# Kernel tuning notes

Hardware: AMD Instinct MI355X
Metric: run time of the kernel (lower is better)

Reference implementation:

```python
import jax, jax.numpy as jnp
import numpy as np

B, S, M, D, F, H = 1, 2048, 512, 1024, 4096, 16
DH = D // H
W = 256  # Longformer half-window: query attends to keys within +/-W global positions


def layer_norm(x, g, b, eps=1e-5):
    mu = jnp.mean(x, axis=-1, keepdims=True)
    var = jnp.var(x, axis=-1, keepdims=True)
    return (x - mu) * jax.lax.rsqrt(var + eps) * g + b


def rel_sinusoid(dists, d_model):
    # Transformer-XL sinusoidal embedding of (possibly negative) relative distances
    inv_freq = 1.0 / (10000.0 ** (jnp.arange(0, d_model, 2, dtype=jnp.float32) / d_model))
    ang = dists[:, None].astype(jnp.float32) * inv_freq[None, :]
    return jnp.concatenate([jnp.sin(ang), jnp.cos(ang)], axis=-1)  # [nR, D]


def setup_inputs() -> dict:
    key = jax.random.key(0)
    ks = jax.random.split(key, 18)
    sc = D ** -0.5
    inp = {
        "x": jax.random.normal(ks[0], (B, S, D), jnp.float32),
        "mem": jax.random.normal(ks[1], (B, M, D), jnp.float32),
        "Wq": jax.random.normal(ks[2], (D, D), jnp.float32) * sc,
        "Wk": jax.random.normal(ks[3], (D, D), jnp.float32) * sc,
        "Wv": jax.random.normal(ks[4], (D, D), jnp.float32) * sc,
        "Wo": jax.random.normal(ks[5], (D, D), jnp.float32) * sc,
        "Wr": jax.random.normal(ks[6], (D, D), jnp.float32) * sc,
        "u": jax.random.normal(ks[7], (H, DH), jnp.float32) * 0.02,
        "v": jax.random.normal(ks[8], (H, DH), jnp.float32) * 0.02,
        "ln1_g": jnp.ones((D,), jnp.float32),
        "ln1_b": jnp.zeros((D,), jnp.float32),
        "W1": jax.random.normal(ks[9], (D, F), jnp.float32) * sc,
        "b1": jnp.zeros((F,), jnp.float32),
        "W2": jax.random.normal(ks[10], (F, D), jnp.float32) * (F ** -0.5),
        "b2": jnp.zeros((D,), jnp.float32),
        "ln2_g": jnp.ones((D,), jnp.float32),
        "ln2_b": jnp.zeros((D,), jnp.float32),
    }
    return inp


def reference(x, mem, Wq, Wk, Wv, Wo, Wr, u, v, ln1_g, ln1_b, W1, b1, W2, b2, ln2_g, ln2_b):
    L = M + S  # key/value length after prepending XL memory
    kv = jnp.concatenate([mem, x], axis=1)  # [B, L, D]
    q = (x @ Wq).reshape(B, S, H, DH)
    k = (kv @ Wk).reshape(B, L, H, DH)
    vv = (kv @ Wv).reshape(B, L, H, DH)

    # relative distances: global query pos = M+i, key pos = j -> dist = M+i-j in [-(S-1), M+S-1]
    dists = jnp.arange(-(S - 1), M + S)  # [nR]
    R = (rel_sinusoid(dists, D) @ Wr).reshape(-1, H, DH)  # [nR, H, DH]

    AC = jnp.einsum("bqhd,blhd->bhql", q + u, k)          # content term
    BD_all = jnp.einsum("bqhd,rhd->bhqr", q + v, R)        # position term per distance
    qi = jnp.arange(S)[:, None]
    kj = jnp.arange(L)[None, :]
    dist = M + qi - kj                                       # [S, L]
    idx = dist + (S - 1)
    BD = jnp.take_along_axis(BD_all, jnp.broadcast_to(idx[None, None], (B, H, S, L)), axis=-1)

    scores = (AC + BD) * (DH ** -0.5)
    band = jnp.abs(dist) <= W                                # sliding-window (banded) mask
    scores = jnp.where(band[None, None], scores, -1e30)
    attn = jax.nn.softmax(scores, axis=-1)
    o = jnp.einsum("bhql,blhd->bqhd", attn, vv).reshape(B, S, D) @ Wo

    h = layer_norm(x + o, ln1_g, ln1_b)                      # residual + LN (dropout: eval mode)
    f = jax.nn.gelu(h @ W1 + b1) @ W2 + b2                   # FFN
    return layer_norm(h + f, ln2_g, ln2_b)
```

## Files before the change

### kernel.cpp

```cpp
#include <hip/hip_runtime.h>
#include <hip/hip_bf16.h>
#include <cstdint>

#define S_ 2048
#define M_ 512
#define L_ 2560
#define D_ 1024
#define F_ 4096
#define H_ 16
#define DH_ 64
#define W_ 256
#define NR_ 513
#define NRP_ 640

typedef unsigned int uint32;
typedef __attribute__((ext_vector_type(8))) short bf16x8;
typedef __attribute__((ext_vector_type(4))) float f32x4;

__device__ __forceinline__ ushort f2bf(float f) {
  uint32 u = __builtin_bit_cast(uint32, f);
  u += 0x7FFFu + ((u >> 16) & 1u);
  return (ushort)(u >> 16);
}
__device__ __forceinline__ float bf2f(ushort s) {
  uint32 u = ((uint32)s) << 16;
  return __builtin_bit_cast(float, u);
}
__device__ __forceinline__ ushort4 pack4(float4 vf) {
  ushort4 r;
  r.x = f2bf(vf.x); r.y = f2bf(vf.y); r.z = f2bf(vf.z); r.w = f2bf(vf.w);
  return r;
}
__device__ __forceinline__ float gelu_tanh(float x) {
  float t = 0.7978845608028654f * x * (1.f + 0.044715f * x * x);
  float e = __expf(2.f * t);
  float th = 1.f - 2.f / (e + 1.f);
  return 0.5f * x * (1.f + th);
}

__device__ __forceinline__ void gld_lds16(const ushort* g, ushort* l) {
  __builtin_amdgcn_global_load_lds((const __attribute__((address_space(1))) void*)g,
                                   (__attribute__((address_space(3))) void*)l, 16, 0, 0);
}

__device__ __forceinline__ void tr_tile(const float* __restrict__ in, ushort* __restrict__ out,
                                        int R, int C, int c0, int r0, int tx, int ty,
                                        float (*tile)[33]) {
#pragma unroll
  for (int i = 0; i < 4; i++)
    tile[ty + i * 8][tx] = in[(size_t)(r0 + ty + i * 8) * C + c0 + tx];
  __syncthreads();
#pragma unroll
  for (int i = 0; i < 4; i++)
    out[(size_t)(c0 + ty + i * 8) * R + r0 + tx] = f2bf(tile[tx][ty + i * 8]);
}

__global__ __launch_bounds__(256)
void prep_kernel(const float* __restrict__ x, const float* __restrict__ mem,
                 const float* __restrict__ Wq, const float* __restrict__ Wk,
                 const float* __restrict__ Wv, const float* __restrict__ Wo,
                 const float* __restrict__ Wr, const float* __restrict__ W1,
                 const float* __restrict__ W2,
                 ushort* __restrict__ WqT, ushort* __restrict__ WkT,
                 ushort* __restrict__ WvT, ushort* __restrict__ WoT,
                 ushort* __restrict__ WrT, ushort* __restrict__ W1T,
                 ushort* __restrict__ W2T,
                 ushort* __restrict__ kvb, ushort* __restrict__ remb) {
  __shared__ float tile[32][33];
  const int bid = blockIdx.x;
  const int tid = threadIdx.x;
  const int tx = tid & 31, ty = tid >> 5;

  if (bid < 5120) {
    const int which = bid >> 10, idx = bid & 1023;
    const float* ins[5] = {Wq, Wk, Wv, Wo, Wr};
    ushort* outs[5] = {WqT, WkT, WvT, WoT, WrT};
    tr_tile(ins[which], outs[which], 1024, 1024, (idx & 31) * 32, (idx >> 5) * 32, tx, ty, tile);
  } else if (bid < 9216) {
    const int idx = bid - 5120;
    tr_tile(W1, W1T, 1024, 4096, (idx % 128) * 32, (idx / 128) * 32, tx, ty, tile);
  } else if (bid < 13312) {
    const int idx = bid - 9216;
    tr_tile(W2, W2T, 4096, 1024, (idx & 31) * 32, (idx >> 5) * 32, tx, ty, tile);
  } else if (bid < 15872) {
    const int k = (bid - 13312) * 256 + tid;
    const int l = k >> 8, c = k & 255;
    const float4* src = (l < M_) ? (const float4*)(mem + (size_t)l * D_)
                                 : (const float4*)(x + (size_t)(l - M_) * D_);
    ((ushort4*)kvb)[k] = pack4(src[c]);
  } else {
    const int idx = (bid - 15872) * 256 + tid;
    const int r = idx >> 9, f = idx & 511;
    if (r < NR_) {
      float invf = expf(-(float)f * (9.210340371976184f / 512.0f));
      float ang = (float)(r - W_) * invf;
      remb[(size_t)r * D_ + f] = f2bf(sinf(ang));
      remb[(size_t)r * D_ + 512 + f] = f2bf(cosf(ang));
    } else if (r < NRP_) {
      remb[(size_t)r * D_ + f] = 0;
      remb[(size_t)r * D_ + 512 + f] = 0;
    }
  }
}

template <int EPI, int SPLITK>
__device__ __forceinline__
void gemm8p2_core(const ushort* __restrict__ A, const ushort* __restrict__ BT,
                  void* __restrict__ Cout, void* __restrict__ Cout2,
                  void* __restrict__ Cout3, void* __restrict__ Cout4,
                  const float* __restrict__ bias, int Msz, int Nsz, int Ksz, int Kstride,
                  int gx, int bid, int nwg, char* dyn) {
  const int tid = threadIdx.x;
  const int wave = tid >> 6, lane = tid & 63;
  const int wr = wave >> 2, wc = wave & 3;
  const int fr = lane & 15, gf = lane >> 4;
  const int sl = fr & 7;

  const int xcd = bid & 7, idx = bid >> 3;
  const int q = nwg >> 3, r8 = nwg & 7;
  const int swz = (xcd < r8 ? xcd * (q + 1) : r8 * (q + 1) + (xcd - r8) * q) + idx;
  const int gy = Msz / 128;
  const int bx = swz % gx;
  const int rest = swz / gx;
  const int by = rest % gy;
  const int bz = rest / gy;
  const int brow = by * 128, bcol = bx * 256;
  const int koff = (SPLITK > 1) ? bz * Ksz : 0;

  const int nt = Ksz >> 6;

  const int srow = tid >> 3;
  const int scol = ((tid & 7) ^ (srow & 7)) * 8;
  const ushort* Ab = A + (size_t)(brow + srow) * Kstride + koff + scol;
  const ushort* Bb = BT + (size_t)(bcol + srow) * Kstride + koff + scol;

  auto stageA = [&](int t, int qm) {
    gld_lds16(Ab + (size_t)(qm * 64) * Kstride + t * 64,
              (ushort*)(dyn + (t & 1) * 49152 + qm * 8192) + wave * 512);
  };
  auto stageB = [&](int t, int qn) {
#pragma unroll
    for (int j = 0; j < 2; j++)
      gld_lds16(Bb + (size_t)(qn * 128 + j * 64) * Kstride + t * 64,
                (ushort*)(dyn + (t & 1) * 49152 + 16384 + qn * 16384 + j * 8192) + wave * 512);
  };

  const int ar0 = (wr * 32 + fr) * 128;
  const int ar1 = (wr * 32 + 16 + fr) * 128;
  const int br0 = (wc * 32 + fr) * 128;
  const int br1 = (wc * 32 + 16 + fr) * 128;
  const int s0 = (gf ^ sl) * 16;
  const int s1 = ((4 + gf) ^ sl) * 16;

  f32x4 acc00[2][2] = {}, acc01[2][2] = {}, acc10[2][2] = {}, acc11[2][2] = {};

  stageA(0, 0); stageB(0, 0); stageB(0, 1); stageA(0, 1);
  stageA(1, 0); stageB(1, 0);
  asm volatile("s_waitcnt vmcnt(3)" ::: "memory");
  __builtin_amdgcn_s_barrier();
  __builtin_amdgcn_sched_barrier(0);

#define PH4(QM, QN, ACC, STAGES, WAITS)                                                 \
  {                                                                                     \
    const char* ab = dyn + cur * 49152 + (QM) * 8192;                                   \
    const char* bb = dyn + cur * 49152 + 16384 + (QN) * 16384;                          \
    bf16x8 a00 = *(const bf16x8*)(ab + ar0 + s0);                                       \
    bf16x8 a10 = *(const bf16x8*)(ab + ar1 + s0);                                       \
    bf16x8 a01 = *(const bf16x8*)(ab + ar0 + s1);                                       \
    bf16x8 a11 = *(const bf16x8*)(ab + ar1 + s1);                                       \
    bf16x8 b00 = *(const bf16x8*)(bb + br0 + s0);                                       \
    bf16x8 b10 = *(const bf16x8*)(bb + br1 + s0);                                       \
    bf16x8 b01 = *(const bf16x8*)(bb + br0 + s1);                                       \
    bf16x8 b11 = *(const bf16x8*)(bb + br1 + s1);                                       \
    STAGES;                                                                             \
    WAITS;                                                                              \
    __builtin_amdgcn_s_barrier();                                                       \
    asm volatile("s_waitcnt lgkmcnt(0)" ::: "memory");                                  \
    __builtin_amdgcn_sched_barrier(0);                                                  \
    __builtin_amdgcn_s_setprio(1);                                                      \
    ACC[0][0] = __builtin_amdgcn_mfma_f32_16x16x32_bf16(a00, b00, ACC[0][0], 0, 0, 0);  \
    ACC[0][1] = __builtin_amdgcn_mfma_f32_16x16x32_bf16(a00, b10, ACC[0][1], 0, 0, 0);  \
    ACC[1][0] = __builtin_amdgcn_mfma_f32_16x16x32_bf16(a10, b00, ACC[1][0], 0, 0, 0);  \
    ACC[1][1] = __builtin_amdgcn_mfma_f32_16x16x32_bf16(a10, b10, ACC[1][1], 0, 0, 0);  \
    ACC[0][0] = __builtin_amdgcn_mfma_f32_16x16x32_bf16(a01, b01, ACC[0][0], 0, 0, 0);  \
    ACC[0][1] = __builtin_amdgcn_mfma_f32_16x16x32_bf16(a01, b11, ACC[0][1], 0, 0, 0);  \
    ACC[1][0] = __builtin_amdgcn_mfma_f32_16x16x32_bf16(a11, b01, ACC[1][0], 0, 0, 0);  \
    ACC[1][1] = __builtin_amdgcn_mfma_f32_16x16x32_bf16(a11, b11, ACC[1][1], 0, 0, 0);  \
    __builtin_amdgcn_s_setprio(0);                                                      \
    __builtin_amdgcn_s_barrier();                                                       \
  }

  for (int t = 0; t < nt; t++) {
    const int cur = t & 1;
    PH4(0, 0, acc00, { if (t + 1 < nt) stageB(t + 1, 1); }, {});
    PH4(0, 1, acc01, { if (t + 1 < nt) stageA(t + 1, 1); }, {});
    PH4(1, 0, acc10, { if (t + 2 < nt) stageA(t + 2, 0); }, {});
    PH4(1, 1, acc11, { if (t + 2 < nt) stageB(t + 2, 0); },
        {
          if (t + 1 < nt) {
            if (t + 2 < nt) asm volatile("s_waitcnt vmcnt(3)" ::: "memory");
            else            asm volatile("s_waitcnt vmcnt(0)" ::: "memory");
          }
        });
  }
#undef PH4

  const int r4 = gf * 4;
  float* co = (float*)Cout;
  bool addb = (EPI == 3);
  if constexpr (SPLITK >= 2) {
    if (bz == 1) { co = (float*)Cout2; addb = false; }
  }
  if constexpr (SPLITK == 4) {
    if (bz == 2) { co = (float*)Cout3; addb = false; }
    if (bz == 3) { co = (float*)Cout4; addb = false; }
  }
  auto wrq = [&](const f32x4 (&ACC)[2][2], int QM, int QN) {
#pragma unroll
    for (int m = 0; m < 2; m++) {
#pragma unroll
      for (int n = 0; n < 2; n++) {
        const int col = bcol + QN * 128 + wc * 32 + n * 16 + fr;
        const int row0 = brow + QM * 64 + wr * 32 + m * 16 + r4;
        if constexpr (EPI == 5) {
          if (col < 1024) {
#pragma unroll
            for (int r = 0; r < 4; r++)
              ((ushort*)Cout)[(size_t)(row0 + r) * 1024 + col] = f2bf(ACC[m][n][r]);
          } else {
            ushort4 pk;
            pk.x = f2bf(ACC[m][n][0]); pk.y = f2bf(ACC[m][n][1]);
            pk.z = f2bf(ACC[m][n][2]); pk.w = f2bf(ACC[m][n][3]);
            *(ushort4*)((ushort*)Cout2 + (size_t)(col - 1024) * Msz + row0) = pk;
          }
        } else if constexpr (EPI == 0 || EPI == 2) {
#pragma unroll
          for (int r = 0; r < 4; r++) {
            float val = ACC[m][n][r];
            size_t o = (size_t)(row0 + r) * Nsz + col;
            if constexpr (EPI == 2) ((ushort*)Cout)[o] = f2bf(gelu_tanh(val + bias[col]));
            else ((ushort*)Cout)[o] = f2bf(val);
          }
        } else {
#pragma unroll
          for (int r = 0; r < 4; r++) {
            float val = ACC[m][n][r];
            co[(size_t)(row0 + r) * Nsz + col] = addb ? val + bias[col] : val;
          }
        }
      }
    }
  };
  wrq(acc00, 0, 0);
  wrq(acc01, 0, 1);
  wrq(acc10, 1, 0);
  wrq(acc11, 1, 1);
}

template <int EPI, int SPLITK>
__global__ __launch_bounds__(512)
void gemm8p2_kern(const ushort* __restrict__ A, const ushort* __restrict__ BT,
                  void* __restrict__ Cout, void* __restrict__ Cout2,
                  void* __restrict__ Cout3, void* __restrict__ Cout4,
                  const float* __restrict__ bias, int Msz, int Nsz, int Ksz, int Kstride,
                  int gx) {
  extern __shared__ __align__(16) char dyn[];
  gemm8p2_core<EPI, SPLITK>(A, BT, Cout, Cout2, Cout3, Cout4, bias,
                            Msz, Nsz, Ksz, Kstride, gx, blockIdx.x, gridDim.x, dyn);
}

__global__ __launch_bounds__(512)
void proj8p(const ushort* __restrict__ kvb, const ushort* __restrict__ WqT,
            const ushort* __restrict__ WkvT, const ushort* __restrict__ WrT,
            const ushort* __restrict__ remb,
            ushort* __restrict__ qb, ushort* __restrict__ kb,
            ushort* __restrict__ Vt, ushort* __restrict__ Rb) {
  extern __shared__ __align__(16) char dyn[];
  const int bid = blockIdx.x;
  if (bid < 64) {
    gemm8p2_core<0, 1>(kvb + 512 * 1024, WqT, qb, nullptr, nullptr, nullptr, nullptr,
                       2048, 1024, 1024, 1024, 4, bid, 64, dyn);
  } else if (bid < 224) {
    gemm8p2_core<5, 1>(kvb, WkvT, kb, Vt, nullptr, nullptr, nullptr,
                       2560, 2048, 1024, 1024, 8, bid - 64, 160, dyn);
  } else {
    gemm8p2_core<0, 1>(remb, WrT, Rb, nullptr, nullptr, nullptr, nullptr,
                       640, 1024, 1024, 1024, 4, bid - 224, 20, dyn);
  }
}

__global__ __launch_bounds__(256)
void attn_mfma5(const ushort* __restrict__ qb, const ushort* __restrict__ kb,
                const ushort* __restrict__ Vt, const ushort* __restrict__ Rb,
                const float* __restrict__ ubias, const float* __restrict__ vbias,
                ushort* __restrict__ attb) {
  const int bid = blockIdx.x;
  const int swz = (bid & 7) * 64 + (bid >> 3);
  const int h = swz >> 5;
  const int i0 = (swz & 31) * 64;
  const int tid = threadIdx.x;
  const int wave = tid >> 6, lane = tid & 63;
  const int g = lane >> 4, fr = lane & 15;
  const int hD = h * DH_;

  __shared__ __align__(16) ushort ring[4][16][128];
  __shared__ __align__(16) ushort Pl[4][16][40];

  const int qi = i0 + wave * 16 + fr;
  bf16x8 afu[2], afv[2];
#pragma unroll
  for (int kst = 0; kst < 2; kst++) {
    const int dof = kst * 32 + g * 8;
    bf16x8 qv = *(const bf16x8*)(qb + (size_t)qi * D_ + hD + dof);
    const float* up = ubias + hD + dof;
    const float* vp = vbias + hD + dof;
    bf16x8 au, av;
#pragma unroll
    for (int j = 0; j < 8; j++) {
      float q = bf2f((ushort)qv[j]);
      au[j] = (short)f2bf(q + up[j]);
      av[j] = (short)f2bf(q + vp[j]);
    }
    afu[kst] = au; afv[kst] = av;
  }

  const int jb = 256 + i0;
  const int smax = 2303 - i0;
  const int sbase = wave * 16;

  auto produce = [&](int r0, bf16x8 rf0, bf16x8 rf1) {
    f32x4 acc = {};
    __builtin_amdgcn_s_setprio(1);
    acc = __builtin_amdgcn_mfma_f32_16x16x32_bf16(afv[0], rf0, acc, 0, 0, 0);
    acc = __builtin_amdgcn_mfma_f32_16x16x32_bf16(afv[1], rf1, acc, 0, 0, 0);
    __builtin_amdgcn_s_setprio(0);
#pragma unroll
    for (int rr = 0; rr < 4; rr++)
      ring[wave][g * 4 + rr][(r0 + fr) & 127] = f2bf(acc[rr]);
  };
  auto loadRrow = [&](int row, bf16x8* out0, bf16x8* out1) {
    const int rc = row < 0 ? 0 : row;
    *out0 = *(const bf16x8*)(Rb + (size_t)rc * D_ + hD + g * 8);
    *out1 = *(const bf16x8*)(Rb + (size_t)rc * D_ + hD + 32 + g * 8);
  };
  auto loadK = [&](int ch, bf16x8 (&kp)[2][2]) {
#pragma unroll
    for (int half = 0; half < 2; half++) {
      const int sa = sbase + ch * 32 + half * 16 + fr;
      const int jc = (jb + sa < L_ - 1) ? (jb + sa) : (L_ - 1);
      kp[half][0] = *(const bf16x8*)(kb + (size_t)jc * 1024 + hD + g * 8);
      kp[half][1] = *(const bf16x8*)(kb + (size_t)jc * 1024 + hD + 32 + g * 8);
    }
  };
  auto loadV = [&](int ch, bf16x8 (&vp)[4]) {
    int kc = jb + sbase + ch * 32 + g * 8;
    if (kc > L_ - 8) kc = L_ - 8;
#pragma unroll
    for (int n = 0; n < 4; n++)
      vp[n] = *(const bf16x8*)(Vt + (size_t)(hD + n * 16 + fr) * L_ + kc);
  };

#pragma unroll
  for (int t = 0; t < 3; t++) {
    const int r0 = 480 + t * 16;
    bf16x8 rf0, rf1;
    loadRrow(r0 + fr, &rf0, &rf1);
    produce(r0, rf0, rf1);
  }

  float m4[4], l4[4];
  f32x4 oacc[4] = {};
#pragma unroll
  for (int rr = 0; rr < 4; rr++) { m4[rr] = -1e30f; l4[rr] = 0.f; }

  bf16x8 kA[2][2], vA[4], kB[2][2], vB[4];
  bf16x8 rA[4], rB[4];
  loadRrow(448 + fr, &rA[0], &rA[1]);
  loadRrow(464 + fr, &rA[2], &rA[3]);
  loadK(0, kA); loadV(0, vA);

  auto body = [&](int ch, bf16x8 (&kU)[2][2], bf16x8 (&vU)[4],
                  bf16x8 (&kP)[2][2], bf16x8 (&vP)[4],
                  bf16x8 (&rU)[4], bf16x8 (&rP)[4], bool first) -> bool {
    const int c0 = sbase + ch * 32;
    if (c0 > smax) return false;
    f32x4 sc[2];
#pragma unroll
    for (int half = 0; half < 2; half++) {
      f32x4 acc = {};
      __builtin_amdgcn_s_setprio(1);
      acc = __builtin_amdgcn_mfma_f32_16x16x32_bf16(afu[0], kU[half][0], acc, 0, 0, 0);
      acc = __builtin_amdgcn_mfma_f32_16x16x32_bf16(afu[1], kU[half][1], acc, 0, 0, 0);
      __builtin_amdgcn_s_setprio(0);
      sc[half] = acc;
    }
    if (ch < 16) {
      loadK(ch + 1, kP);
      loadV(ch + 1, vP);
    }
    if (ch < 15) {
      loadRrow(416 - ch * 32 + fr, &rP[0], &rP[1]);
      loadRrow(432 - ch * 32 + fr, &rP[2], &rP[3]);
    }
#pragma unroll
    for (int half = 0; half < 2; half++) {
      const int rb2 = 512 + g * 4 - (ch * 32 + half * 16 + fr);
      const int sa = c0 + half * 16 + fr;
#pragma unroll
      for (int rr = 0; rr < 4; rr++) {
        const int r = rb2 + rr;
        const float bd = bf2f(ring[wave][g * 4 + rr][r & 127]);
        const bool valid = ((unsigned)r <= 512u) && (sa <= smax);
        sc[half][rr] = valid ? (sc[half][rr] + bd) * 0.125f : -1e30f;
      }
    }
    if (first) {
      f32x4 cm;
#pragma unroll
      for (int rr = 0; rr < 4; rr++) cm[rr] = fmaxf(sc[0][rr], sc[1][rr]);
#pragma unroll
      for (int off = 8; off; off >>= 1)
#pragma unroll
        for (int rr = 0; rr < 4; rr++) cm[rr] = fmaxf(cm[rr], __shfl_xor(cm[rr], off));
#pragma unroll
      for (int rr = 0; rr < 4; rr++) m4[rr] = cm[rr];
    } else {
      bool rise = false;
#pragma unroll
      for (int rr = 0; rr < 4; rr++)
        rise |= (fmaxf(sc[0][rr], sc[1][rr]) > m4[rr] + 8.f);
      if (__any(rise)) {
        f32x4 cm;
#pragma unroll
        for (int rr = 0; rr < 4; rr++) cm[rr] = fmaxf(sc[0][rr], sc[1][rr]);
#pragma unroll
        for (int off = 8; off; off >>= 1)
#pragma unroll
          for (int rr = 0; rr < 4; rr++) cm[rr] = fmaxf(cm[rr], __shfl_xor(cm[rr], off));
#pragma unroll
        for (int rr = 0; rr < 4; rr++) {
          const float nm = fmaxf(m4[rr], cm[rr]);
          const float esc = __expf(m4[rr] - nm);
          m4[rr] = nm;
          l4[rr] *= esc;
#pragma unroll
          for (int n = 0; n < 4; n++) oacc[n][rr] *= esc;
        }
      }
    }
    f32x4 pA, pB;
#pragma unroll
    for (int rr = 0; rr < 4; rr++) {
      pA[rr] = __expf(sc[0][rr] - m4[rr]);
      pB[rr] = __expf(sc[1][rr] - m4[rr]);
      l4[rr] += pA[rr] + pB[rr];
    }
#pragma unroll
    for (int rr = 0; rr < 4; rr++) {
      Pl[wave][g * 4 + rr][fr]      = f2bf(pA[rr]);
      Pl[wave][g * 4 + rr][16 + fr] = f2bf(pB[rr]);
    }
    bf16x8 pf = *(const bf16x8*)&Pl[wave][fr][g * 8];
    if (ch < 16) {
      produce(448 - ch * 32, rU[0], rU[1]);
      produce(464 - ch * 32, rU[2], rU[3]);
    }
    __builtin_amdgcn_s_setprio(1);
#pragma unroll
    for (int n = 0; n < 4; n++)
      oacc[n] = __builtin_amdgcn_mfma_f32_16x16x32_bf16(pf, vU[n], oacc[n], 0, 0, 0);
    __builtin_amdgcn_s_setprio(0);
    return true;
  };

  bool cont = body(0, kA, vA, kB, vB, rA, rB, true);
  for (int ch = 1; ch < 17 && cont; ch += 2) {
    cont = body(ch, kB, vB, kA, vA, rB, rA, false);
    if (!cont || ch + 1 >= 17) break;
    cont = body(ch + 1, kA, vA, kB, vB, rA, rB, false);
  }

#pragma unroll
  for (int off = 8; off; off >>= 1)
#pragma unroll
    for (int rr = 0; rr < 4; rr++) l4[rr] += __shfl_xor(l4[rr], off);
#pragma unroll
  for (int rr = 0; rr < 4; rr++) {
    const float inv = 1.f / l4[rr];
    const size_t rowo = (size_t)(i0 + sbase + g * 4 + rr) * D_ + hD;
#pragma unroll
    for (int n = 0; n < 4; n++)
      attb[rowo + n * 16 + fr] = f2bf(oacc[n][rr] * inv);
  }
}

__global__ __launch_bounds__(256)
void ln_kernel(const float* __restrict__ a, const float* __restrict__ b,
               const float* __restrict__ c, const float* __restrict__ d,
               const float* __restrict__ e,
               const float* __restrict__ gamma, const float* __restrict__ beta,
               float* __restrict__ outf, ushort* __restrict__ outb) {
  const int row = blockIdx.x;
  const int tid = threadIdx.x;
  const int wave = tid >> 6, lane = tid & 63;
  float4 va = ((const float4*)(a + (size_t)row * D_))[tid];
  float4 vb4 = ((const float4*)(b + (size_t)row * D_))[tid];
  float4 xv;
  xv.x = va.x + vb4.x; xv.y = va.y + vb4.y; xv.z = va.z + vb4.z; xv.w = va.w + vb4.w;
  if (c) {
    float4 vc = ((const float4*)(c + (size_t)row * D_))[tid];
    xv.x += vc.x; xv.y += vc.y; xv.z += vc.z; xv.w += vc.w;
  }
  if (d) {
    float4 vd = ((const float4*)(d + (size_t)row * D_))[tid];
    xv.x += vd.x; xv.y += vd.y; xv.z += vd.z; xv.w += vd.w;
  }
  if (e) {
    float4 ve = ((const float4*)(e + (size_t)row * D_))[tid];
    xv.x += ve.x; xv.y += ve.y; xv.z += ve.z; xv.w += ve.w;
  }
  float s = xv.x + xv.y + xv.z + xv.w;
  float q = xv.x * xv.x + xv.y * xv.y + xv.z * xv.z + xv.w * xv.w;
#pragma unroll
  for (int off = 32; off; off >>= 1) { s += __shfl_xor(s, off); q += __shfl_xor(q, off); }
  __shared__ float red[8];
  if (lane == 0) { red[wave * 2] = s; red[wave * 2 + 1] = q; }
  __syncthreads();
  float ts = red[0] + red[2] + red[4] + red[6];
  float tq = red[1] + red[3] + red[5] + red[7];
  float mu = ts * (1.f / D_);
  float var = tq * (1.f / D_) - mu * mu;
  float rs = rsqrtf(var + 1e-5f);
  float4 g4 = ((const float4*)gamma)[tid];
  float4 be4 = ((const float4*)beta)[tid];
  float4 y;
  y.x = (xv.x - mu) * rs * g4.x + be4.x;
  y.y = (xv.y - mu) * rs * g4.y + be4.y;
  y.z = (xv.z - mu) * rs * g4.z + be4.z;
  y.w = (xv.w - mu) * rs * g4.w + be4.w;
  ((float4*)(outf + (size_t)row * D_))[tid] = y;
  if (outb) ((ushort4*)(outb + (size_t)row * D_))[tid] = pack4(y);
}

extern "C" void kernel_launch(void* const* d_in, const int* in_sizes, int n_in,
                              void* d_out, int out_size, void* d_ws, size_t ws_size,
                              hipStream_t stream) {
  const float* x    = (const float*)d_in[0];
  const float* mem  = (const float*)d_in[1];
  const float* Wq   = (const float*)d_in[2];
  const float* Wk   = (const float*)d_in[3];
  const float* Wv   = (const float*)d_in[4];
  const float* Wo   = (const float*)d_in[5];
  const float* Wr   = (const float*)d_in[6];
  const float* u    = (const float*)d_in[7];
  const float* v    = (const float*)d_in[8];
  const float* ln1g = (const float*)d_in[9];
  const float* ln1b = (const float*)d_in[10];
  const float* W1   = (const float*)d_in[11];
  const float* b1   = (const float*)d_in[12];
  const float* W2   = (const float*)d_in[13];
  const float* b2   = (const float*)d_in[14];
  const float* ln2g = (const float*)d_in[15];
  const float* ln2b = (const float*)d_in[16];
  float* out = (float*)d_out;

  char* ws = (char*)d_ws;
  size_t off = 0;
  auto take = [&](size_t n) { char* p = ws + off; off += (n + 255) & ~(size_t)255; return p; };

  ushort* WqT = (ushort*)take(2097152);
  ushort* WkT = (ushort*)take(2097152);
  ushort* WvT = (ushort*)take(2097152);
  ushort* WoT = (ushort*)take(2097152);
  ushort* WrT = (ushort*)take(2097152);
  ushort* W1T = (ushort*)take(8388608);
  ushort* W2T = (ushort*)take(8388608);

  char* regA = take(8388608);
  ushort* kvb  = (ushort*)regA;
  ushort* remb = (ushort*)(regA + 5242880);
  float*  fbuf = (float*)regA;

  char* regB = take(20185088);
  ushort* qb   = (ushort*)regB;
  ushort* kb   = (ushort*)(regB + 4194304);
  ushort* Vt   = (ushort*)(regB + 9437184);
  ushort* Rb   = (ushort*)(regB + 14680064);
  ushort* attb = (ushort*)(regB + 15990784);
  float*  o2b  = (float*)regB;
  ushort* g    = (ushort*)regB;

  float*  o2 = (float*)take(8388608);
  float*  h  = (float*)take(8388608);
  ushort* hb = (ushort*)take(4194304);

  float* p2 = (float*)WqT;
  float* p3 = (float*)W1T;

  prep_kernel<<<17152, 256, 0, stream>>>(x, mem, Wq, Wk, Wv, Wo, Wr, W1, W2,
                                         WqT, WkT, WvT, WoT, WrT, W1T, W2T, kvb, remb);

  proj8p<<<244, 512, 98304, stream>>>(kvb, WqT, WkT, WrT, remb, qb, kb, Vt, Rb);

  attn_mfma5<<<512, 256, 0, stream>>>(qb, kb, Vt, Rb, u, v, attb);

  gemm8p2_kern<1, 2><<<128, 512, 98304, stream>>>(attb, WoT, o2, o2b, nullptr, nullptr,
                                                  nullptr, 2048, 1024, 512, 1024, 4);
  ln_kernel<<<2048, 256, 0, stream>>>(x, o2, o2b, nullptr, nullptr, ln1g, ln1b, h, hb);

  gemm8p2_kern<2, 1><<<256, 512, 98304, stream>>>(hb, W1T, g, nullptr, nullptr, nullptr,
                                                  b1, 2048, 4096, 1024, 1024, 16);

  gemm8p2_kern<3, 4><<<256, 512, 98304, stream>>>(g, W2T, fbuf, o2, p2, p3,
                                                  b2, 2048, 1024, 1024, 4096, 4);
  ln_kernel<<<2048, 256, 0, stream>>>(h, fbuf, o2, p2, p3, ln2g, ln2b, out, nullptr);
}
```

Baseline: 187.9 us.

## Split attention key range across two blocks and merge partial softmax results

The banded attention kernel now launches twice as many blocks, each covering half of the key chunks, and writes unnormalized fp32 partial outputs plus running max and sum. A new merge kernel rescales and combines the two halves, normalizes, and emits bf16. The aim is more blocks in flight on a 512-block grid that underfills the GPU, so the serial chunk loop per block gets shorter. The cost is extra fp32 global traffic, a second launch, and a small LDS padding change to the ring buffer.

```diff
diff --git a/kernel.cpp b/kernel.cpp
--- a/kernel.cpp
+++ b/kernel.cpp
@@ -290,12 +290,15 @@
 }
 
 __global__ __launch_bounds__(256)
-void attn_mfma5(const ushort* __restrict__ qb, const ushort* __restrict__ kb,
+void attn_mfma6(const ushort* __restrict__ qb, const ushort* __restrict__ kb,
                 const ushort* __restrict__ Vt, const ushort* __restrict__ Rb,
                 const float* __restrict__ ubias, const float* __restrict__ vbias,
-                ushort* __restrict__ attb) {
+                float* __restrict__ OA, float* __restrict__ OB,
+                float* __restrict__ mlb) {
   const int bid = blockIdx.x;
-  const int swz = (bid & 7) * 64 + (bid >> 3);
+  const int hf = bid >> 9;
+  const int inner = bid & 511;
+  const int swz = (inner & 7) * 64 + (inner >> 3);
   const int h = swz >> 5;
   const int i0 = (swz & 31) * 64;
   const int tid = threadIdx.x;
@@ -303,7 +306,10 @@
   const int g = lane >> 4, fr = lane & 15;
   const int hD = h * DH_;
 
-  __shared__ __align__(16) ushort ring[4][16][128];
+  const int chS = hf ? 9 : 0;
+  const int chE = hf ? 16 : 8;
+
+  __shared__ __align__(16) ushort ring[4][16][136];
   __shared__ __align__(16) ushort Pl[4][16][40];
 
   const int qi = i0 + wave * 16 + fr;
@@ -360,9 +366,10 @@
       vp[n] = *(const bf16x8*)(Vt + (size_t)(hD + n * 16 + fr) * L_ + kc);
   };
 
+  const int base = 480 - chS * 32;
 #pragma unroll
   for (int t = 0; t < 3; t++) {
-    const int r0 = 480 + t * 16;
+    const int r0 = base + t * 16;
     bf16x8 rf0, rf1;
     loadRrow(r0 + fr, &rf0, &rf1);
     produce(r0, rf0, rf1);
@@ -375,9 +382,9 @@
 
   bf16x8 kA[2][2], vA[4], kB[2][2], vB[4];
   bf16x8 rA[4], rB[4];
-  loadRrow(448 + fr, &rA[0], &rA[1]);
-  loadRrow(464 + fr, &rA[2], &rA[3]);
-  loadK(0, kA); loadV(0, vA);
+  loadRrow(base - 32 + fr, &rA[0], &rA[1]);
+  loadRrow(base - 16 + fr, &rA[2], &rA[3]);
+  loadK(chS, kA); loadV(chS, vA);
 
   auto body = [&](int ch, bf16x8 (&kU)[2][2], bf16x8 (&vU)[4],
                   bf16x8 (&kP)[2][2], bf16x8 (&vP)[4],
@@ -394,11 +401,11 @@
       __builtin_amdgcn_s_setprio(0);
       sc[half] = acc;
     }
-    if (ch < 16) {
+    if (ch < chE) {
       loadK(ch + 1, kP);
       loadV(ch + 1, vP);
     }
-    if (ch < 15) {
+    if (ch < chE - 1) {
       loadRrow(416 - ch * 32 + fr, &rP[0], &rP[1]);
       loadRrow(432 - ch * 32 + fr, &rP[2], &rP[3]);
     }
@@ -461,7 +468,7 @@
       Pl[wave][g * 4 + rr][16 + fr] = f2bf(pB[rr]);
     }
     bf16x8 pf = *(const bf16x8*)&Pl[wave][fr][g * 8];
-    if (ch < 16) {
+    if (ch < chE) {
       produce(448 - ch * 32, rU[0], rU[1]);
       produce(464 - ch * 32, rU[2], rU[3]);
     }
@@ -473,10 +480,10 @@
     return true;
   };
 
-  bool cont = body(0, kA, vA, kB, vB, rA, rB, true);
-  for (int ch = 1; ch < 17 && cont; ch += 2) {
+  bool cont = body(chS, kA, vA, kB, vB, rA, rB, true);
+  for (int ch = chS + 1; ch <= chE && cont; ch += 2) {
     cont = body(ch, kB, vB, kA, vA, rB, rA, false);
-    if (!cont || ch + 1 >= 17) break;
+    if (!cont || ch + 1 > chE) break;
     cont = body(ch + 1, kA, vA, kB, vB, rA, rB, false);
   }
 
@@ -484,14 +491,44 @@
   for (int off = 8; off; off >>= 1)
 #pragma unroll
     for (int rr = 0; rr < 4; rr++) l4[rr] += __shfl_xor(l4[rr], off);
+
+  float* Obuf = hf ? OB : OA;
+  float* ml = mlb + (hf ? 65536 : 0);
 #pragma unroll
   for (int rr = 0; rr < 4; rr++) {
-    const float inv = 1.f / l4[rr];
-    const size_t rowo = (size_t)(i0 + sbase + g * 4 + rr) * D_ + hD;
+    const int row = i0 + sbase + g * 4 + rr;
+    const size_t rowo = (size_t)row * D_ + hD;
 #pragma unroll
     for (int n = 0; n < 4; n++)
-      attb[rowo + n * 16 + fr] = f2bf(oacc[n][rr] * inv);
-  }
+      Obuf[rowo + n * 16 + fr] = oacc[n][rr];
+    if (fr == 0) {
+      ml[row * 16 + h] = m4[rr];
+      ml[32768 + row * 16 + h] = l4[rr];
+    }
+  }
+}
+
+__global__ __launch_bounds__(256)
+void attn_merge(const float* __restrict__ OA, const float* __restrict__ OB,
+                const float* __restrict__ mlb, ushort* __restrict__ attb) {
+  const int q = blockIdx.x;
+  const int tid = threadIdx.x;
+  const int h = tid >> 4;
+  const float mA = mlb[q * 16 + h];
+  const float lA = mlb[32768 + q * 16 + h];
+  const float mB = mlb[65536 + q * 16 + h];
+  const float lB = mlb[98304 + q * 16 + h];
+  const float m = fmaxf(mA, mB);
+  const float eA = __expf(mA - m), eB = __expf(mB - m);
+  const float inv = 1.f / (eA * lA + eB * lB);
+  float4 a = ((const float4*)(OA + (size_t)q * 1024))[tid];
+  float4 b = ((const float4*)(OB + (size_t)q * 1024))[tid];
+  ushort4 o;
+  o.x = f2bf((a.x * eA + b.x * eB) * inv);
+  o.y = f2bf((a.y * eA + b.y * eB) * inv);
+  o.z = f2bf((a.z * eA + b.z * eB) * inv);
+  o.w = f2bf((a.w * eA + b.w * eB) * inv);
+  ((ushort4*)(attb + (size_t)q * 1024))[tid] = o;
 }
 
 __global__ __launch_bounds__(256)
@@ -596,13 +633,17 @@
 
   float* p2 = (float*)WqT;
   float* p3 = (float*)W1T;
+  float* OA = o2;
+  float* OB = h;
+  float* mlb = (float*)hb;
 
   prep_kernel<<<17152, 256, 0, stream>>>(x, mem, Wq, Wk, Wv, Wo, Wr, W1, W2,
                                          WqT, WkT, WvT, WoT, WrT, W1T, W2T, kvb, remb);
 
   proj8p<<<244, 512, 98304, stream>>>(kvb, WqT, WkT, WrT, remb, qb, kb, Vt, Rb);
 
-  attn_mfma5<<<512, 256, 0, stream>>>(qb, kb, Vt, Rb, u, v, attb);
+  attn_mfma6<<<1024, 256, 0, stream>>>(qb, kb, Vt, Rb, u, v, OA, OB, mlb);
+  attn_merge<<<2048, 256, 0, stream>>>(OA, OB, mlb, attb);
 
   gemm8p2_kern<1, 2><<<128, 512, 98304, stream>>>(attb, WoT, o2, o2b, nullptr, nullptr,
                                                   nullptr, 2048, 1024, 512, 1024, 4);
```

Result: slower. 195.9 us (+4.3%).
